# Performance work log

Measured on AMD Instinct MI355X. Metric: run time of the kernel, lower is better.

Reference implementation:

```python
import jax, jax.numpy as jnp
import numpy as np

B, S, D, H = 4, 2048, 1024, 16
DK = D // H

def setup_inputs() -> dict:
    key = jax.random.key(0)
    ks = jax.random.split(key, 11)
    scale = 1.0 / np.sqrt(D)
    inp = {
        'q': jax.random.normal(ks[0], (B, S, D), jnp.float32),
        'k': jax.random.normal(ks[1], (B, S, D), jnp.float32),
        'v': jax.random.normal(ks[2], (B, S, D), jnp.float32),
        'Wq': jax.random.normal(ks[3], (D, D), jnp.float32) * scale,
        'bq': jnp.zeros((D,), jnp.float32),
        'Wk': jax.random.normal(ks[4], (D, D), jnp.float32) * scale,
        'bk': jnp.zeros((D,), jnp.float32),
        'Wv': jax.random.normal(ks[5], (D, D), jnp.float32) * scale,
        'bv': jnp.zeros((D,), jnp.float32),
        'Wo': jax.random.normal(ks[6], (D, D), jnp.float32) * scale,
        'bo': jnp.zeros((D,), jnp.float32),
        # diagonal mask: 0 on the diagonal (self position masked out), 1 elsewhere
        'mask': (1 - jnp.eye(S, dtype=jnp.int32))[None, None, :, :],
    }
    return inp


def reference(q, k, v, Wq, bq, Wk, bk, Wv, bv, Wo, bo, mask):
    def proj(x, W, b):
        # [B,S,D] -> [B,H,S,DK]
        y = x @ W.T + b
        return y.reshape(B, S, H, DK).transpose(0, 2, 1, 3)

    qh = proj(q, Wq, bq)
    kh = proj(k, Wk, bk)
    vh = proj(v, Wv, bv)

    scores = jnp.einsum('bhsd,bhtd->bhst', qh, kh) / jnp.sqrt(jnp.float32(DK))
    scores = jnp.where(mask == 0, jnp.finfo(scores.dtype).min, scores)
    attn = jax.nn.softmax(scores, axis=-1)  # dropout is identity in eval mode
    out = jnp.einsum('bhst,bhtd->bhsd', attn, vh)
    out = out.transpose(0, 2, 1, 3).reshape(B, S, D)
    return out @ Wo.T + bo
```

## Files before the change

### kernel.cpp

```cpp
#include <hip/hip_runtime.h>
#include <stdint.h>

#define S_LEN 2048
#define D_DIM 1024
#define NB 4
#define NH 16
#define DKH 64
#define M_ROWS (NB * S_LEN)
#define PLD 72

typedef float  f32x4 __attribute__((ext_vector_type(4)));
typedef short  s16x8 __attribute__((ext_vector_type(8)));
typedef unsigned short u16;
typedef u16    u16x4 __attribute__((ext_vector_type(4)));

#define AS1 __attribute__((address_space(1)))
#define AS3 __attribute__((address_space(3)))

__device__ __forceinline__ void gload16(const u16* g, u16* l) {
    __builtin_amdgcn_global_load_lds((const AS1 void*)g, (AS3 void*)l, 16, 0, 0);
}

__device__ __forceinline__ u16 f2bf(float f) {
    uint32_t u = __builtin_bit_cast(uint32_t, f);
    return (u16)((u + 0x7fffu + ((u >> 16) & 1u)) >> 16);
}
__device__ __forceinline__ u16 f2bf_cheap(float f) {
    uint32_t u = __builtin_bit_cast(uint32_t, f);
    return (u16)((u + 0x8000u) >> 16);
}

__global__ __launch_bounds__(256) void conv_kernel(const float* __restrict__ src,
                                                   u16* __restrict__ dst, int n)
{
    int i = (blockIdx.x * 256 + threadIdx.x) * 8;
    if (i + 8 > n) return;
    f32x4 a = *(const f32x4*)(src + i);
    f32x4 b = *(const f32x4*)(src + i + 4);
    s16x8 r;
#pragma unroll
    for (int j = 0; j < 4; ++j) r[j]     = (short)f2bf(a[j]);
#pragma unroll
    for (int j = 0; j < 4; ++j) r[j + 4] = (short)f2bf(b[j]);
    *(s16x8*)(dst + i) = r;
}

__global__ __launch_bounds__(256) void conv2_kernel(const float* __restrict__ a,
                                                    const float* __restrict__ b,
                                                    u16* __restrict__ da,
                                                    u16* __restrict__ db)
{
    const float* src = blockIdx.z ? b : a;
    u16* dst        = blockIdx.z ? db : da;
    int i = (blockIdx.x * 256 + threadIdx.x) * 8;
    f32x4 lo = *(const f32x4*)(src + i);
    f32x4 hi = *(const f32x4*)(src + i + 4);
    s16x8 r;
#pragma unroll
    for (int j = 0; j < 4; ++j) r[j]     = (short)f2bf(lo[j]);
#pragma unroll
    for (int j = 0; j < 4; ++j) r[j + 4] = (short)f2bf(hi[j]);
    *(s16x8*)(dst + i) = r;
}

__global__ __launch_bounds__(256) void conv3_kernel(const float* __restrict__ a,
                                                    const float* __restrict__ b,
                                                    const float* __restrict__ c,
                                                    u16* __restrict__ dst)
{
    const int z = blockIdx.z;
    const float* src = (z == 0) ? a : (z == 1) ? b : c;
    int i = (blockIdx.x * 256 + threadIdx.x) * 8;
    f32x4 lo = *(const f32x4*)(src + i);
    f32x4 hi = *(const f32x4*)(src + i + 4);
    s16x8 r;
#pragma unroll
    for (int j = 0; j < 4; ++j) r[j]     = (short)f2bf(lo[j]);
#pragma unroll
    for (int j = 0; j < 4; ++j) r[j + 4] = (short)f2bf(hi[j]);
    *(s16x8*)(dst + (size_t)z * (D_DIM * D_DIM) + i) = r;
}

__device__ __forceinline__ void stage_tile(const u16* __restrict__ X,
                                           const u16* __restrict__ Wt,
                                           int m0, int n0, int k0,
                                           u16* As, u16* Bs, int tid, int wv)
{
#pragma unroll
    for (int i = 0; i < 4; ++i) {
        const int c   = tid + i * 256;
        const int row = c >> 3;
        const int sg  = (c & 7) ^ (row & 7);
        const int lb  = (i * 256 + wv * 64) * 8;
        gload16(&X [(size_t)(m0 + row) * D_DIM + k0 + sg * 8], &As[lb]);
        gload16(&Wt[(size_t)(n0 + row) * D_DIM + k0 + sg * 8], &Bs[lb]);
    }
}

__device__ __forceinline__ void compute_tile(const u16* As, const u16* Bs,
                                             f32x4 acc[4][4],
                                             int wm, int wn, int ln, int quad, int l7)
{
#pragma unroll
    for (int ks = 0; ks < 2; ++ks) {
        const int sA = ((ks * 4 + quad) ^ l7) * 8;
        s16x8 af[4], bfr[4];
#pragma unroll
        for (int t = 0; t < 4; ++t) {
            af[t]  = *(const s16x8*)&As[(wm * 64 + t * 16 + ln) * 64 + sA];
            bfr[t] = *(const s16x8*)&Bs[(wn * 64 + t * 16 + ln) * 64 + sA];
        }
#pragma unroll
        for (int tM = 0; tM < 4; ++tM)
#pragma unroll
            for (int tN = 0; tN < 4; ++tN)
                acc[tM][tN] = __builtin_amdgcn_mfma_f32_16x16x32_bf16(
                    af[tM], bfr[tN], acc[tM][tN], 0, 0, 0);
    }
}

__device__ __forceinline__ void gemm128_body(const u16* __restrict__ X,
                                             const u16* __restrict__ Wt,
                                             int m0, int n0,
                                             u16* As, u16* Bs,
                                             f32x4 acc[4][4])
{
    const int tid  = threadIdx.x;
    const int wv   = tid >> 6;
    const int lane = tid & 63;
    const int ln   = lane & 15;
    const int quad = lane >> 4;
    const int wm   = wv >> 1;
    const int wn   = wv & 1;
    const int l7   = ln & 7;

    for (int k0 = 0; k0 < D_DIM; k0 += 64) {
        __syncthreads();
        stage_tile(X, Wt, m0, n0, k0, As, Bs, tid, wv);
        __syncthreads();
        compute_tile(As, Bs, acc, wm, wn, ln, quad, l7);
    }
}

__device__ __forceinline__ void gemm128_dbuf(const u16* __restrict__ X,
                                             const u16* __restrict__ Wt,
                                             int m0, int n0,
                                             u16* As0, u16* Bs0,
                                             u16* As1, u16* Bs1,
                                             f32x4 acc[4][4])
{
    const int tid  = threadIdx.x;
    const int wv   = tid >> 6;
    const int lane = tid & 63;
    const int ln   = lane & 15;
    const int quad = lane >> 4;
    const int wm   = wv >> 1;
    const int wn   = wv & 1;
    const int l7   = ln & 7;

    stage_tile(X, Wt, m0, n0, 0, As0, Bs0, tid, wv);
    __syncthreads();
    for (int t = 0; t < 16; t += 2) {
        stage_tile(X, Wt, m0, n0, (t + 1) * 64, As1, Bs1, tid, wv);
        compute_tile(As0, Bs0, acc, wm, wn, ln, quad, l7);
        __syncthreads();
        if (t + 2 < 16)
            stage_tile(X, Wt, m0, n0, (t + 2) * 64, As0, Bs0, tid, wv);
        compute_tile(As1, Bs1, acc, wm, wn, ln, quad, l7);
        __syncthreads();
    }
}

__global__ __launch_bounds__(256) void qk_kernel(
    const u16* __restrict__ xq, const u16* __restrict__ xk,
    const u16* __restrict__ Wb,
    const float* __restrict__ bq, const float* __restrict__ bk,
    u16* __restrict__ Qh, u16* __restrict__ Kh)
{
    __shared__ __attribute__((aligned(16))) u16 As[128 * 64];
    __shared__ __attribute__((aligned(16))) u16 Bs[128 * 64];

    const int mode = blockIdx.z;
    const u16* X        = mode ? xk : xq;
    const u16* Wt       = Wb + (size_t)mode * (D_DIM * D_DIM);
    const float* bias   = mode ? bk : bq;
    u16* dst            = mode ? Kh : Qh;
    const float qscale  = mode ? 1.0f : 0.18033688011112042f;

    const int lin = blockIdx.y * 8 + blockIdx.x;
    const int swz = (lin & 7) * 64 + (lin >> 3);
    const int n0  = (swz & 7) * 128;
    const int m0  = (swz >> 3) * 128;

    f32x4 zero = {0.f, 0.f, 0.f, 0.f};
    f32x4 acc[4][4];
#pragma unroll
    for (int i = 0; i < 4; ++i)
#pragma unroll
        for (int j = 0; j < 4; ++j) acc[i][j] = zero;

    gemm128_body(X, Wt, m0, n0, As, Bs, acc);

    const int tid  = threadIdx.x;
    const int wv   = tid >> 6;
    const int lane = tid & 63;
    const int ln   = lane & 15;
    const int quad = lane >> 4;
    const int wm   = wv >> 1;
    const int wn   = wv & 1;

#pragma unroll
    for (int tM = 0; tM < 4; ++tM) {
#pragma unroll
        for (int tN = 0; tN < 4; ++tN) {
            const int ng = n0 + wn * 64 + tN * 16 + ln;
            const float bf32 = bias[ng];
            const int h  = ng >> 6;
            const int dk = ng & 63;
            const int mbase = m0 + wm * 64 + tM * 16 + quad * 4;
            const int b = mbase >> 11;
            const int s = mbase & 2047;
#pragma unroll
            for (int r = 0; r < 4; ++r)
                dst[((size_t)(b * NH + h) * S_LEN + (s + r)) * DKH + dk] =
                    f2bf((acc[tM][tN][r] + bf32) * qscale);
        }
    }
}

__global__ __launch_bounds__(256) void vproj_kernel(
    const u16* __restrict__ xv, const u16* __restrict__ Wv2,
    const float* __restrict__ bv, u16* __restrict__ Vt)
{
    __shared__ __attribute__((aligned(16))) u16 As0[128 * 64];
    __shared__ __attribute__((aligned(16))) u16 Bs0[128 * 64];
    __shared__ __attribute__((aligned(16))) u16 As1[128 * 64];
    __shared__ __attribute__((aligned(16))) u16 Bs1[128 * 64];

    const int lin = blockIdx.y * 8 + blockIdx.x;
    const int swz = (lin & 7) * 64 + (lin >> 3);
    const int n0  = (swz & 7) * 128;
    const int m0  = (swz >> 3) * 128;

    f32x4 zero = {0.f, 0.f, 0.f, 0.f};
    f32x4 acc[4][4];
#pragma unroll
    for (int i = 0; i < 4; ++i)
#pragma unroll
        for (int j = 0; j < 4; ++j) acc[i][j] = zero;

    gemm128_dbuf(xv, Wv2, m0, n0, As0, Bs0, As1, Bs1, acc);

    const int tid  = threadIdx.x;
    const int wv   = tid >> 6;
    const int lane = tid & 63;
    const int ln   = lane & 15;
    const int quad = lane >> 4;
    const int wm   = wv >> 1;
    const int wn   = wv & 1;

#pragma unroll
    for (int tM = 0; tM < 4; ++tM) {
#pragma unroll
        for (int tN = 0; tN < 4; ++tN) {
            const int ng = n0 + wn * 64 + tN * 16 + ln;
            const float bf32 = bv[ng];
            const int h  = ng >> 6;
            const int dk = ng & 63;
            const int mbase = m0 + wm * 64 + tM * 16 + quad * 4;
            const int b = mbase >> 11;
            const int s = mbase & 2047;
            u16x4 pk;
#pragma unroll
            for (int r = 0; r < 4; ++r) pk[r] = f2bf(acc[tM][tN][r] + bf32);
            *(u16x4*)&Vt[((size_t)((b * NH + h) * DKH + dk)) * S_LEN + s] = pk;
        }
    }
}

__global__ __launch_bounds__(256) void attn_kernel(
    const u16* __restrict__ Qh, const u16* __restrict__ Kh,
    const u16* __restrict__ Vt, u16* __restrict__ ctx)
{
    __shared__ __attribute__((aligned(16))) u16 Ks[64 * 64];
    __shared__ __attribute__((aligned(16))) u16 Vs[64 * 64];
    __shared__ __attribute__((aligned(16))) u16 QPs[64 * PLD];

    const int tid  = threadIdx.x;
    const int wv   = tid >> 6;
    const int lane = tid & 63;
    const int ln   = lane & 15;
    const int quad = lane >> 4;
    const int l7   = ln & 7;

    const int lin = blockIdx.y * 32 + blockIdx.x;
    const int xcd = lin & 7;
    const int t_  = lin >> 3;
    const int bh  = xcd * 8 + (t_ >> 5);
    const int q0  = (t_ & 31) * 64;

    const size_t qkbase = (size_t)bh * S_LEN * DKH;
    const size_t vbase  = (size_t)bh * DKH * S_LEN;

#pragma unroll
    for (int i = 0; i < 2; ++i) {
        const int c = tid + i * 256, row = c >> 3;
        const int sg = (c & 7) ^ (row & 7);
        gload16(&Qh[qkbase + (size_t)(q0 + row) * DKH + sg * 8],
                &QPs[(i * 256 + wv * 64) * 8]);
    }
    __syncthreads();

    s16x8 aq[2];
#pragma unroll
    for (int ks = 0; ks < 2; ++ks)
        aq[ks] = *(const s16x8*)&QPs[(wv * 16 + ln) * 64 + (((ks * 4 + quad) ^ l7) * 8)];

    float l_part[4] = {0.f, 0.f, 0.f, 0.f};
    f32x4 zero = {0.f, 0.f, 0.f, 0.f};
    f32x4 o_acc[4] = {zero, zero, zero, zero};

    const int rbase = q0 + wv * 16 + quad * 4;
    const int rowA = wv * 16 + ln;
    const int rotA = (((rowA >> 2) & 7)) * 8;
    const int rotW = ((4 * wv + quad) & 7) * 8;

    for (int kb = 0; kb < S_LEN; kb += 64) {
        __syncthreads();
#pragma unroll
        for (int i = 0; i < 2; ++i) {
            const int c = tid + i * 256, row = c >> 3;
            const int sg = (c & 7) ^ (row & 7);
            const int lb = (i * 256 + wv * 64) * 8;
            gload16(&Kh[qkbase + (size_t)(kb + row) * DKH + sg * 8], &Ks[lb]);
            gload16(&Vt[vbase + (size_t)row * S_LEN + kb + sg * 8], &Vs[lb]);
        }
        __syncthreads();

        f32x4 sf[4];
#pragma unroll
        for (int nt = 0; nt < 4; ++nt) {
            f32x4 acc = zero;
#pragma unroll
            for (int ks = 0; ks < 2; ++ks) {
                s16x8 bk_ = *(const s16x8*)&Ks[(nt * 16 + ln) * 64 + (((ks * 4 + quad) ^ l7) * 8)];
                acc = __builtin_amdgcn_mfma_f32_16x16x32_bf16(aq[ks], bk_, acc, 0, 0, 0);
            }
            sf[nt] = acc;
        }

        if (kb == q0) {
#pragma unroll
            for (int nt = 0; nt < 4; ++nt)
#pragma unroll
                for (int r = 0; r < 4; ++r) {
                    float p = __builtin_amdgcn_exp2f(sf[nt][r]);
                    if (rbase + r == kb + nt * 16 + ln) p = 0.f;
                    sf[nt][r] = p;
                    l_part[r] += p;
                }
        } else {
#pragma unroll
            for (int nt = 0; nt < 4; ++nt)
#pragma unroll
                for (int r = 0; r < 4; ++r) {
                    float p = __builtin_amdgcn_exp2f(sf[nt][r]);
                    sf[nt][r] = p;
                    l_part[r] += p;
                }
        }

#pragma unroll
        for (int nt = 0; nt < 4; ++nt)
#pragma unroll
            for (int r = 0; r < 4; ++r) {
                int row  = wv * 16 + quad * 4 + r;
                int col  = ((nt * 16 + ln) + rotW) & 63;
                QPs[row * PLD + col] = f2bf_cheap(sf[nt][r]);
            }

#pragma unroll
        for (int ks = 0; ks < 2; ++ks) {
            int colA = ((ks * 32 + quad * 8) + rotA) & 63;
            s16x8 ap = *(const s16x8*)&QPs[rowA * PLD + colA];
#pragma unroll
            for (int nt = 0; nt < 4; ++nt) {
                s16x8 bvv = *(const s16x8*)&Vs[(nt * 16 + ln) * 64 + (((ks * 4 + quad) ^ l7) * 8)];
                o_acc[nt] = __builtin_amdgcn_mfma_f32_16x16x32_bf16(ap, bvv, o_acc[nt], 0, 0, 0);
            }
        }
    }

#pragma unroll
    for (int r = 0; r < 4; ++r) {
#pragma unroll
        for (int off = 1; off < 16; off <<= 1)
            l_part[r] += __shfl_xor(l_part[r], off, 16);
    }

    const int b = bh >> 4;
    const int h = bh & 15;
#pragma unroll
    for (int nt = 0; nt < 4; ++nt) {
#pragma unroll
        for (int r = 0; r < 4; ++r) {
            float val = o_acc[nt][r] / l_part[r];
            int sg = q0 + wv * 16 + quad * 4 + r;
            ctx[((size_t)b * S_LEN + sg) * D_DIM + h * DKH + nt * 16 + ln] = f2bf(val);
        }
    }
}

__global__ __launch_bounds__(256) void oproj128_kernel(
    const u16* __restrict__ ctx, const u16* __restrict__ WoB,
    const float* __restrict__ bo, float* __restrict__ out, float sentinel)
{
    __shared__ __attribute__((aligned(16))) u16 As0[128 * 64];
    __shared__ __attribute__((aligned(16))) u16 Bs0[128 * 64];
    __shared__ __attribute__((aligned(16))) u16 As1[128 * 64];
    __shared__ __attribute__((aligned(16))) u16 Bs1[128 * 64];

    const int lin = blockIdx.y * 8 + blockIdx.x;
    const int swz = (lin & 7) * 64 + (lin >> 3);
    const int n0  = (swz & 7) * 128;
    const int m0  = (swz >> 3) * 128;

    f32x4 zero = {0.f, 0.f, 0.f, 0.f};
    f32x4 acc[4][4];
#pragma unroll
    for (int i = 0; i < 4; ++i)
#pragma unroll
        for (int j = 0; j < 4; ++j) acc[i][j] = zero;

    gemm128_dbuf(ctx, WoB, m0, n0, As0, Bs0, As1, Bs1, acc);

    const int tid  = threadIdx.x;
    const int wv   = tid >> 6;
    const int lane = tid & 63;
    const int ln   = lane & 15;
    const int quad = lane >> 4;
    const int wm   = wv >> 1;
    const int wn   = wv & 1;

#pragma unroll
    for (int tM = 0; tM < 4; ++tM) {
#pragma unroll
        for (int tN = 0; tN < 4; ++tN) {
            const int ng = n0 + wn * 64 + tN * 16 + ln;
            const float bf32 = bo[ng];
            const int mbase = m0 + wm * 64 + tM * 16 + quad * 4;
#pragma unroll
            for (int r = 0; r < 4; ++r) {
                float val = acc[tM][tN][r] + bf32;
                if (mbase + r == 0 && ng == 0) val += sentinel;
                out[(size_t)(mbase + r) * D_DIM + ng] = val;
            }
        }
    }
}

extern "C" void kernel_launch(void* const* d_in, const int* in_sizes, int n_in,
                              void* d_out, int out_size, void* d_ws, size_t ws_size,
                              hipStream_t stream)
{
    const float* q  = (const float*)d_in[0];
    const float* k  = (const float*)d_in[1];
    const float* v  = (const float*)d_in[2];
    const float* Wq = (const float*)d_in[3];
    const float* bq = (const float*)d_in[4];
    const float* Wk = (const float*)d_in[5];
    const float* bk = (const float*)d_in[6];
    const float* Wv = (const float*)d_in[7];
    const float* bv = (const float*)d_in[8];
    const float* Wo = (const float*)d_in[9];
    const float* bo = (const float*)d_in[10];

    const size_t headSz = (size_t)NB * NH * S_LEN * DKH;
    const int    WN     = D_DIM * D_DIM;
    u16* Qh  = (u16*)d_ws;
    u16* Kh  = Qh + headSz;
    u16* Vt  = Kh + headSz;
    u16* ctx = Vt + headSz;
    u16* Wb  = (u16*)d_out;
    u16* xk  = Wb + 3 * WN;
    u16* WoB = Qh;
    float* out = (float*)d_out;

    float sentinel = 0.f;
    {
        const int expect[12] = {8388608, 8388608, 8388608, 1048576, 1024, 1048576,
                                1024, 1048576, 1024, 1048576, 1024, 4194304};
        bool ok = (n_in == 12);
        for (int i = 0; ok && i < 12; ++i) ok = (in_sizes[i] == expect[i]);
        if (!ok)                               sentinel = 1000.f;
        else if (ws_size < 4 * headSz * 2)     sentinel = 2000.f;
        else if (out_size != (int)headSz)      sentinel = 3000.f;
    }

    conv3_kernel<<<dim3(WN / 2048, 1, 3), 256, 0, stream>>>(Wq, Wk, Wv, Wb);

    conv_kernel<<<dim3((int)(headSz / 2048)), 256, 0, stream>>>(v, ctx, (int)headSz);
    vproj_kernel<<<dim3(8, 64), 256, 0, stream>>>(ctx, Wb + 2 * WN, bv, Vt);

    conv2_kernel<<<dim3((int)(headSz / 2048), 1, 2), 256, 0, stream>>>(q, k, ctx, xk);
    qk_kernel<<<dim3(8, 64, 2), 256, 0, stream>>>(ctx, xk, Wb, bq, bk, Qh, Kh);

    attn_kernel<<<dim3(S_LEN / 64, NB * NH), 256, 0, stream>>>(Qh, Kh, Vt, ctx);

    conv_kernel<<<dim3(WN / 2048), 256, 0, stream>>>(Wo, WoB, WN);

    oproj128_kernel<<<dim3(8, 64), 256, 0, stream>>>(ctx, WoB, bo, out, sentinel);
}
```

Before: 386.0 us.

## Merge input conversions, use counter-based GEMM pipeline, split attention launch

Three fp32-to-bf16 input conversions now run in one launch, with v staged in the Qh buffer so vproj no longer waits on its own conversion. The double-buffered GEMM loop is rewritten with explicit vmcnt/lgkmcnt waits and raw s_barrier, so the next tile's global-to-LDS loads stay in flight during compute. Attention is split into two launches over half the batch-heads each, with a base offset parameter. Each change saves launch or sync overhead but relies on hand-written waitcnt values that must match the number of loads issued.

```diff
diff --git a/kernel.cpp b/kernel.cpp
--- a/kernel.cpp
+++ b/kernel.cpp
@@ -45,28 +45,10 @@
     *(s16x8*)(dst + i) = r;
 }
 
-__global__ __launch_bounds__(256) void conv2_kernel(const float* __restrict__ a,
-                                                    const float* __restrict__ b,
-                                                    u16* __restrict__ da,
-                                                    u16* __restrict__ db)
-{
-    const float* src = blockIdx.z ? b : a;
-    u16* dst        = blockIdx.z ? db : da;
-    int i = (blockIdx.x * 256 + threadIdx.x) * 8;
-    f32x4 lo = *(const f32x4*)(src + i);
-    f32x4 hi = *(const f32x4*)(src + i + 4);
-    s16x8 r;
-#pragma unroll
-    for (int j = 0; j < 4; ++j) r[j]     = (short)f2bf(lo[j]);
-#pragma unroll
-    for (int j = 0; j < 4; ++j) r[j + 4] = (short)f2bf(hi[j]);
-    *(s16x8*)(dst + i) = r;
-}
-
-__global__ __launch_bounds__(256) void conv3_kernel(const float* __restrict__ a,
-                                                    const float* __restrict__ b,
-                                                    const float* __restrict__ c,
-                                                    u16* __restrict__ dst)
+__global__ __launch_bounds__(256) void conv3w_kernel(const float* __restrict__ a,
+                                                     const float* __restrict__ b,
+                                                     const float* __restrict__ c,
+                                                     u16* __restrict__ dst)
 {
     const int z = blockIdx.z;
     const float* src = (z == 0) ? a : (z == 1) ? b : c;
@@ -79,6 +61,27 @@
 #pragma unroll
     for (int j = 0; j < 4; ++j) r[j + 4] = (short)f2bf(hi[j]);
     *(s16x8*)(dst + (size_t)z * (D_DIM * D_DIM) + i) = r;
+}
+
+__global__ __launch_bounds__(256) void conv3x_kernel(const float* __restrict__ a,
+                                                     const float* __restrict__ b,
+                                                     const float* __restrict__ c,
+                                                     u16* __restrict__ da,
+                                                     u16* __restrict__ db,
+                                                     u16* __restrict__ dc)
+{
+    const int z = blockIdx.z;
+    const float* src = (z == 0) ? a : (z == 1) ? b : c;
+    u16* dst         = (z == 0) ? da : (z == 1) ? db : dc;
+    int i = (blockIdx.x * 256 + threadIdx.x) * 8;
+    f32x4 lo = *(const f32x4*)(src + i);
+    f32x4 hi = *(const f32x4*)(src + i + 4);
+    s16x8 r;
+#pragma unroll
+    for (int j = 0; j < 4; ++j) r[j]     = (short)f2bf(lo[j]);
+#pragma unroll
+    for (int j = 0; j < 4; ++j) r[j + 4] = (short)f2bf(hi[j]);
+    *(s16x8*)(dst + i) = r;
 }
 
 __device__ __forceinline__ void stage_tile(const u16* __restrict__ X,
@@ -142,12 +145,12 @@
     }
 }
 
-__device__ __forceinline__ void gemm128_dbuf(const u16* __restrict__ X,
-                                             const u16* __restrict__ Wt,
-                                             int m0, int n0,
-                                             u16* As0, u16* Bs0,
-                                             u16* As1, u16* Bs1,
-                                             f32x4 acc[4][4])
+__device__ __forceinline__ void gemm128_dbuf_cnt(const u16* __restrict__ X,
+                                                 const u16* __restrict__ Wt,
+                                                 int m0, int n0,
+                                                 u16* As0, u16* Bs0,
+                                                 u16* As1, u16* Bs1,
+                                                 f32x4 acc[4][4])
 {
     const int tid  = threadIdx.x;
     const int wv   = tid >> 6;
@@ -159,15 +162,26 @@
     const int l7   = ln & 7;
 
     stage_tile(X, Wt, m0, n0, 0, As0, Bs0, tid, wv);
-    __syncthreads();
-    for (int t = 0; t < 16; t += 2) {
-        stage_tile(X, Wt, m0, n0, (t + 1) * 64, As1, Bs1, tid, wv);
-        compute_tile(As0, Bs0, acc, wm, wn, ln, quad, l7);
-        __syncthreads();
-        if (t + 2 < 16)
-            stage_tile(X, Wt, m0, n0, (t + 2) * 64, As0, Bs0, tid, wv);
-        compute_tile(As1, Bs1, acc, wm, wn, ln, quad, l7);
-        __syncthreads();
+#pragma unroll
+    for (int t = 0; t < 16; ++t) {
+        u16* Ac = (t & 1) ? As1 : As0;
+        u16* Bc = (t & 1) ? Bs1 : Bs0;
+        u16* An = (t & 1) ? As0 : As1;
+        u16* Bn = (t & 1) ? Bs0 : Bs1;
+        if (t < 15) {
+            stage_tile(X, Wt, m0, n0, (t + 1) * 64, An, Bn, tid, wv);
+            asm volatile("s_waitcnt vmcnt(8)" ::: "memory");
+        } else {
+            asm volatile("s_waitcnt vmcnt(0)" ::: "memory");
+        }
+        __builtin_amdgcn_s_barrier();
+        __builtin_amdgcn_sched_barrier(0);
+        compute_tile(Ac, Bc, acc, wm, wn, ln, quad, l7);
+        if (t < 15) {
+            asm volatile("s_waitcnt lgkmcnt(0)" ::: "memory");
+            __builtin_amdgcn_s_barrier();
+            __builtin_amdgcn_sched_barrier(0);
+        }
     }
 }
 
@@ -249,7 +263,7 @@
 #pragma unroll
         for (int j = 0; j < 4; ++j) acc[i][j] = zero;
 
-    gemm128_dbuf(xv, Wv2, m0, n0, As0, Bs0, As1, Bs1, acc);
+    gemm128_dbuf_cnt(xv, Wv2, m0, n0, As0, Bs0, As1, Bs1, acc);
 
     const int tid  = threadIdx.x;
     const int wv   = tid >> 6;
@@ -280,7 +294,7 @@
 
 __global__ __launch_bounds__(256) void attn_kernel(
     const u16* __restrict__ Qh, const u16* __restrict__ Kh,
-    const u16* __restrict__ Vt, u16* __restrict__ ctx)
+    const u16* __restrict__ Vt, u16* __restrict__ ctx, int bh0)
 {
     __shared__ __attribute__((aligned(16))) u16 Ks[64 * 64];
     __shared__ __attribute__((aligned(16))) u16 Vs[64 * 64];
@@ -296,7 +310,7 @@
     const int lin = blockIdx.y * 32 + blockIdx.x;
     const int xcd = lin & 7;
     const int t_  = lin >> 3;
-    const int bh  = xcd * 8 + (t_ >> 5);
+    const int bh  = bh0 + xcd * 4 + (t_ >> 5);
     const int q0  = (t_ & 31) * 64;
 
     const size_t qkbase = (size_t)bh * S_LEN * DKH;
@@ -432,7 +446,7 @@
 #pragma unroll
         for (int j = 0; j < 4; ++j) acc[i][j] = zero;
 
-    gemm128_dbuf(ctx, WoB, m0, n0, As0, Bs0, As1, Bs1, acc);
+    gemm128_dbuf_cnt(ctx, WoB, m0, n0, As0, Bs0, As1, Bs1, acc);
 
     const int tid  = threadIdx.x;
     const int wv   = tid >> 6;
@@ -483,6 +497,7 @@
     u16* ctx = Vt + headSz;
     u16* Wb  = (u16*)d_out;
     u16* xk  = Wb + 3 * WN;
+    u16* xv  = Qh;
     u16* WoB = Qh;
     float* out = (float*)d_out;
 
@@ -497,15 +512,15 @@
         else if (out_size != (int)headSz)      sentinel = 3000.f;
     }
 
-    conv3_kernel<<<dim3(WN / 2048, 1, 3), 256, 0, stream>>>(Wq, Wk, Wv, Wb);
-
-    conv_kernel<<<dim3((int)(headSz / 2048)), 256, 0, stream>>>(v, ctx, (int)headSz);
-    vproj_kernel<<<dim3(8, 64), 256, 0, stream>>>(ctx, Wb + 2 * WN, bv, Vt);
-
-    conv2_kernel<<<dim3((int)(headSz / 2048), 1, 2), 256, 0, stream>>>(q, k, ctx, xk);
+    conv3w_kernel<<<dim3(WN / 2048, 1, 3), 256, 0, stream>>>(Wq, Wk, Wv, Wb);
+    conv3x_kernel<<<dim3((int)(headSz / 2048), 1, 3), 256, 0, stream>>>(
+        v, q, k, xv, ctx, xk);
+
+    vproj_kernel<<<dim3(8, 64), 256, 0, stream>>>(xv, Wb + 2 * WN, bv, Vt);
     qk_kernel<<<dim3(8, 64, 2), 256, 0, stream>>>(ctx, xk, Wb, bq, bk, Qh, Kh);
 
-    attn_kernel<<<dim3(S_LEN / 64, NB * NH), 256, 0, stream>>>(Qh, Kh, Vt, ctx);
+    attn_kernel<<<dim3(32, 32), 256, 0, stream>>>(Qh, Kh, Vt, ctx, 0);
+    attn_kernel<<<dim3(32, 32), 256, 0, stream>>>(Qh, Kh, Vt, ctx, 32);
 
     conv_kernel<<<dim3(WN / 2048), 256, 0, stream>>>(Wo, WoB, WN);
 
```

Result: no change. 387.0 us (+0.3%).
